# Optimization experiments

Measured on AMD Instinct MI355X. Metric: run time of the kernel, lower is better.

## Reference

```python
import jax, jax.numpy as jnp
import numpy as np

HIDDEN = 64
NUM_LAYERS = 6
BN_EPS = 1e-5


def setup_inputs() -> dict:
    key = jax.random.key(0)
    N, M = 1024, 1024
    num_nodes = N + M
    ks = jax.random.split(key, 12)
    x = jax.random.normal(ks[0], (num_nodes, 2), dtype=jnp.float32)
    # complete bipartite edges: (a, N+b) for all a in [0,N), b in [0,M), row-major so view(N,M) is meaningful
    row = jnp.repeat(jnp.arange(N, dtype=jnp.int64), M)
    col = N + jnp.tile(jnp.arange(M, dtype=jnp.int64), N)
    edge_index = jnp.stack([row, col], axis=0)
    s = 1.0 / np.sqrt(HIDDEN)
    return {
        "x": x,
        "edge_index": edge_index,
        "in_w": jax.random.normal(ks[1], (2, HIDDEN), jnp.float32) * 0.5,
        "in_b": jnp.zeros((HIDDEN,), jnp.float32),
        "conv_w": jax.random.normal(ks[2], (NUM_LAYERS, HIDDEN, HIDDEN), jnp.float32) * s,
        "conv_b": jnp.zeros((NUM_LAYERS, HIDDEN), jnp.float32),
        "bn_gamma": jnp.ones((NUM_LAYERS, HIDDEN), jnp.float32),
        "bn_beta": jnp.zeros((NUM_LAYERS, HIDDEN), jnp.float32),
        "out_w": jax.random.normal(ks[3], (2 * HIDDEN, 1), jnp.float32) * s,
        "out_b": jnp.zeros((1,), jnp.float32),
        "N": N,
        "M": M,
    }


def reference(x, edge_index, in_w, in_b, conv_w, conv_b, bn_gamma, bn_beta, out_w, out_b, N, M):
    num_nodes = x.shape[0]
    # GCN normalization with added self-loops (PyG GCNConv defaults)
    loops = jnp.arange(num_nodes, dtype=edge_index.dtype)
    row = jnp.concatenate([edge_index[0], loops])
    col = jnp.concatenate([edge_index[1], loops])
    deg = jax.ops.segment_sum(jnp.ones_like(col, dtype=x.dtype), col, num_segments=num_nodes)
    dinv = jnp.where(deg > 0, jax.lax.rsqrt(deg), 0.0)
    norm = dinv[row] * dinv[col]  # [E+num_nodes]

    h = jax.nn.relu(x @ in_w + in_b)
    for i in range(NUM_LAYERS):
        h_res = h
        hw = h @ conv_w[i]
        agg = jax.ops.segment_sum(hw[row] * norm[:, None], col, num_segments=num_nodes)
        h = agg + conv_b[i]
        # BatchNorm1d in training mode: batch stats, biased variance
        mu = h.mean(axis=0)
        var = ((h - mu) ** 2).mean(axis=0)
        h = (h - mu) * jax.lax.rsqrt(var + BN_EPS) * bn_gamma[i] + bn_beta[i]
        h = jax.nn.relu(h)
        if i > 0 and i % 2 == 1:
            h = h + h_res

    ef = jnp.concatenate([h[edge_index[0]], h[edge_index[1]]], axis=1)  # [E, 2H]
    scores = (ef @ out_w + out_b)[:, 0]
    return scores.reshape(N, M)
```

## Files before the change

kernel.cpp:

```cpp
#include <hip/hip_runtime.h>


#define NBLK 64
#define MAGIC 0x13572468u

__device__ __forceinline__ float relu_(float x) { return x > 0.f ? x : 0.f; }

#define AT_LOAD(p)    __hip_atomic_load((p), __ATOMIC_RELAXED, __HIP_MEMORY_SCOPE_AGENT)
#define AT_STORE(p,v) __hip_atomic_store((p), (v), __ATOMIC_RELAXED, __HIP_MEMORY_SCOPE_AGENT)
#define AT_ADD(p,v)   __hip_atomic_fetch_add((p), (v), __ATOMIC_RELAXED, __HIP_MEMORY_SCOPE_AGENT)

#define PART_OFF  256
#define UV_OFF    12544
#define FLAG_OFF  14592

__global__ __launch_bounds__(256, 1) void k_fused(
    const float* __restrict__ x,
    const float* __restrict__ in_w, const float* __restrict__ in_b,
    const float* __restrict__ conv_w,
    const float* __restrict__ bn_g, const float* __restrict__ bn_b,
    const float* __restrict__ out_w,
    unsigned int* __restrict__ ws)
{
    __shared__ float Wl[2][4096];
    __shared__ float hl[32 * 68];
    __shared__ float sredS[4 * 64], sredQ[4 * 64];
    __shared__ float stat[256];
    __shared__ float pcoef[64], scoef[64];
    __shared__ float g_lds[384], b_lds[384];
    __shared__ float ow_lds[128];

    const int t = threadIdx.x, b = blockIdx.x;
    const int nl = t >> 3;
    const int fi = t & 7;
    const int f0 = fi * 8;
    const int node = b * 32 + nl;
    const bool isA = b < 32;
    float* part = (float*)(ws + PART_OFF);
    float* uv   = (float*)(ws + UV_OFF);

    {
        const float4* src = (const float4*)conv_w;
        float4* dst = (float4*)Wl[0];
        dst[t]       = src[t];
        dst[t + 256] = src[t + 256];
        dst[t + 512] = src[t + 512];
        dst[t + 768] = src[t + 768];
        for (int i = t; i < 384; i += 256) { g_lds[i] = bn_g[i]; b_lds[i] = bn_b[i]; }
        if (t < 128) ow_lds[t] = out_w[t];
    }

    if (b == 0) {
        for (int i = t; i < 192; i += 256) AT_STORE(ws + i, 0u);
        for (int i = t; i < 12288; i += 256) AT_STORE((unsigned*)part + i, 0u);
        asm volatile("s_waitcnt vmcnt(0)" ::: "memory");
        __syncthreads();
        if (t == 0) AT_STORE(ws + FLAG_OFF, MAGIC);
    }

    {
        float x0 = x[node * 2], x1 = x[node * 2 + 1];
#pragma unroll
        for (int j = 0; j < 8; j++) {
            int f = f0 + j;
            hl[nl * 68 + f] = relu_(fmaf(x0, in_w[f], fmaf(x1, in_w[64 + f], in_b[f])));
        }
    }
    __syncthreads();

    for (int layer = 0; layer < 6; layer++) {
        const float* Wb = Wl[layer & 1];
        float acc[8];
#pragma unroll
        for (int j = 0; j < 8; j++) acc[j] = 0.f;

#pragma unroll 4
        for (int k = 0; k < 64; k += 4) {
            float4 hh = *(const float4*)&hl[nl * 68 + k];
            float hv[4] = {hh.x, hh.y, hh.z, hh.w};
#pragma unroll
            for (int j = 0; j < 4; j++) {
                const float* wr = Wb + (k + j) * 64 + f0;
                float4 w0 = *(const float4*)wr;
                float4 w1 = *(const float4*)(wr + 4);
                float wv[8] = {w0.x, w0.y, w0.z, w0.w, w1.x, w1.y, w1.z, w1.w};
#pragma unroll
                for (int q = 0; q < 8; q++) acc[q] = fmaf(hv[j], wv[q], acc[q]);
            }
        }

        {
            float sv[8], qv[8];
#pragma unroll
            for (int j = 0; j < 8; j++) { sv[j] = acc[j]; qv[j] = acc[j] * acc[j]; }
#pragma unroll
            for (int m = 8; m < 64; m <<= 1) {
#pragma unroll
                for (int j = 0; j < 8; j++) {
                    sv[j] += __shfl_xor(sv[j], m);
                    qv[j] += __shfl_xor(qv[j], m);
                }
            }
            int w = t >> 6, lane = t & 63;
            if (lane < 8) {
#pragma unroll
                for (int j = 0; j < 8; j++) {
                    sredS[w * 64 + lane * 8 + j] = sv[j];
                    sredQ[w * 64 + lane * 8 + j] = qv[j];
                }
            }
        }
        if (layer == 0) {
            __syncthreads();
            if (t == 0) while (AT_LOAD(ws + FLAG_OFF) != MAGIC) {}
        }
        __syncthreads();

        if (t < 64) {
            float S = sredS[t] + sredS[64 + t] + sredS[128 + t] + sredS[192 + t];
            float Q = sredQ[t] + sredQ[64 + t] + sredQ[128 + t] + sredQ[192 + t];
            float* base = part + layer * 2048 + (b & 7) * 256 + (isA ? 0 : 128);
            AT_ADD(base + t, S);
            AT_ADD(base + 64 + t, Q);
        }

        asm volatile("s_waitcnt vmcnt(0)" ::: "memory");
        __syncthreads();
        if (t == 0) AT_ADD(ws + layer * 32, 1u);

        float4 pf0, pf1, pf2, pf3;
        if (layer < 5) {
            const float4* src = (const float4*)(conv_w + (layer + 1) * 4096);
            pf0 = src[t];
            pf1 = src[t + 256];
            pf2 = src[t + 512];
            pf3 = src[t + 768];
        }

        if (t == 0) {
            const unsigned int* c = ws + layer * 32;
            for (;;) {
                unsigned a0 = AT_LOAD(c);
                unsigned a1 = AT_LOAD(c);
                unsigned a2 = AT_LOAD(c);
                unsigned a3 = AT_LOAD(c);
                if (a0 >= NBLK) break;
                if (a1 >= NBLK) break;
                if (a2 >= NBLK) break;
                if (a3 >= NBLK) break;
            }
        }
        __syncthreads();

        {
            int item = t;
            const float* p = part + layer * 2048 + item;
            float s = 0.f;
#pragma unroll
            for (int r = 0; r < 8; r++) s += AT_LOAD(p + r * 256);
            stat[item] = s;
        }

        if (layer < 5) {
            float4* dst = (float4*)Wl[(layer + 1) & 1];
            dst[t]       = pf0;
            dst[t + 256] = pf1;
            dst[t + 512] = pf2;
            dst[t + 768] = pf3;
        }
        __syncthreads();

        if (t < 64) {
            float SA = stat[t], QA = stat[64 + t], SB = stat[128 + t], QB = stat[192 + t];
            const float c1 = 9.75609756097561e-4f;
            const float c2 = 3.1234752377721214e-2f;
            float sumAgg = SA + c1 * SB + 1024.f * c2 * SA;
            float sumSq  = QA + c1 * c1 * QB + 2.f * c1 * c2 * SA * SB
                         + 1024.f * c2 * c2 * SA * SA;
            float meanAgg = sumAgg * (1.f / 2048.f);
            float var = sumSq * (1.f / 2048.f) - meanAgg * meanAgg;
            float rstd = rsqrtf(var + 1e-5f);
            float scale = rstd * g_lds[layer * 64 + t];
            float bt = b_lds[layer * 64 + t];
            if (isA) { pcoef[t] = scale;      scoef[t] = bt - meanAgg * scale; }
            else     { pcoef[t] = c1 * scale; scoef[t] = bt + (c2 * SA - meanAgg) * scale; }
        }
        __syncthreads();

        float vals[8];
#pragma unroll
        for (int j = 0; j < 8; j++)
            vals[j] = relu_(fmaf(acc[j], pcoef[f0 + j], scoef[f0 + j]));
        if (layer == 1 || layer == 3 || layer == 5) {
#pragma unroll
            for (int j = 0; j < 8; j++) vals[j] += hl[nl * 68 + f0 + j];
        }

        if (layer < 5) {
#pragma unroll
            for (int j = 0; j < 8; j++) hl[nl * 68 + f0 + j] = vals[j];
            __syncthreads();
        } else {
            const float* w = ow_lds + (isA ? 0 : 64) + f0;
            float d = 0.f;
#pragma unroll
            for (int j = 0; j < 8; j++) d = fmaf(vals[j], w[j], d);
            d += __shfl_xor(d, 1);
            d += __shfl_xor(d, 2);
            d += __shfl_xor(d, 4);
            if (fi == 0) AT_STORE(uv + node, d);
        }
    }
}

__global__ __launch_bounds__(256) void k_out(const float* __restrict__ uv,
                                             const float* __restrict__ out_b,
                                             float* __restrict__ out) {
    const int a = blockIdx.x;
    const int t = threadIdx.x;
    float ua = uv[a] + out_b[0];
    float4 vv = ((const float4*)(uv + 1024))[t];
    ((float4*)(out + a * 1024))[t] =
        make_float4(ua + vv.x, ua + vv.y, ua + vv.z, ua + vv.w);
}

extern "C" void kernel_launch(void* const* d_in, const int* in_sizes, int n_in,
                              void* d_out, int out_size, void* d_ws, size_t ws_size,
                              hipStream_t stream) {
    const float* x      = (const float*)d_in[0];
    const float* in_w   = (const float*)d_in[2];
    const float* in_b   = (const float*)d_in[3];
    const float* conv_w = (const float*)d_in[4];
    const float* bn_g   = (const float*)d_in[6];
    const float* bn_b   = (const float*)d_in[7];
    const float* out_w  = (const float*)d_in[8];
    const float* out_b  = (const float*)d_in[9];
    float* out = (float*)d_out;

    unsigned int* ws = (unsigned int*)d_ws;
    const float* uv = (const float*)(ws + UV_OFF);

    k_fused<<<NBLK, 256, 0, stream>>>(x, in_w, in_b, conv_w, bn_g, bn_b,
                                      out_w, ws);
    k_out<<<1024, 256, 0, stream>>>(uv, out_b, out);
}
```

Before: 113.7 us.

## Split-K GEMM across waves with LDS reduction and single-wave epilogue

The per-layer 32x64x64 matmul is repartitioned so each wave handles a quarter of the K dimension for all 32 nodes, with each thread covering 4 nodes x 8 features. Waves 1-3 write partial sums to a swizzled LDS buffer, and wave 0 reduces them. Wave 0 alone then computes the BN statistics, issues the global atomics, waits at the grid barrier and applies the epilogue. The hidden-state buffer uses an XOR-swizzled layout instead of padding. The aim is more register reuse of the weight loads and fewer block-wide barriers around the atomics, at the cost of an extra LDS reduction pass and more serialized atomics per thread in a single wave.

```diff
diff --git a/kernel.cpp b/kernel.cpp
--- a/kernel.cpp
+++ b/kernel.cpp
@@ -23,18 +23,21 @@
     unsigned int* __restrict__ ws)
 {
     __shared__ float Wl[2][4096];
-    __shared__ float hl[32 * 68];
-    __shared__ float sredS[4 * 64], sredQ[4 * 64];
+    __shared__ float hl[2048];
+    __shared__ float Pp[3 * 2048];
     __shared__ float stat[256];
-    __shared__ float pcoef[64], scoef[64];
     __shared__ float g_lds[384], b_lds[384];
     __shared__ float ow_lds[128];
 
     const int t = threadIdx.x, b = blockIdx.x;
-    const int nl = t >> 3;
-    const int fi = t & 7;
-    const int f0 = fi * 8;
-    const int node = b * 32 + nl;
+    const int w    = t >> 6;
+    const int lane = t & 63;
+    const int fi   = lane & 7;
+    const int f0   = fi * 8;
+    const int ng   = lane >> 3;
+    const int n0   = ng * 4;
+    const int sw   = ng & 3;
+    const int kb   = w * 16;
     const bool isA = b < 32;
     float* part = (float*)(ws + PART_OFF);
     float* uv   = (float*)(ws + UV_OFF);
@@ -59,40 +62,92 @@
     }
 
     {
+        const int nl = t >> 3, fj = (t & 7) * 8;
+        const int rsw = (nl >> 2) & 3;
+        const int node = b * 32 + nl;
         float x0 = x[node * 2], x1 = x[node * 2 + 1];
 #pragma unroll
         for (int j = 0; j < 8; j++) {
-            int f = f0 + j;
-            hl[nl * 68 + f] = relu_(fmaf(x0, in_w[f], fmaf(x1, in_w[64 + f], in_b[f])));
+            int f = fj + j;
+            float v = relu_(fmaf(x0, in_w[f], fmaf(x1, in_w[64 + f], in_b[f])));
+            hl[nl * 64 + ((((f >> 2)) ^ rsw) << 2) + (f & 3)] = v;
         }
     }
     __syncthreads();
 
     for (int layer = 0; layer < 6; layer++) {
         const float* Wb = Wl[layer & 1];
-        float acc[8];
-#pragma unroll
-        for (int j = 0; j < 8; j++) acc[j] = 0.f;
-
-#pragma unroll 4
-        for (int k = 0; k < 64; k += 4) {
-            float4 hh = *(const float4*)&hl[nl * 68 + k];
-            float hv[4] = {hh.x, hh.y, hh.z, hh.w};
+        float acc[4][8];
+#pragma unroll
+        for (int n = 0; n < 4; n++)
+#pragma unroll
+            for (int j = 0; j < 8; j++) acc[n][j] = 0.f;
+
+#pragma unroll
+        for (int kk = 0; kk < 16; kk += 4) {
+            const int cb = (kb + kk) >> 2;
+            float hv[4][4];
+#pragma unroll
+            for (int n = 0; n < 4; n++) {
+                float4 h4 = *(const float4*)&hl[(n0 + n) * 64 + ((cb ^ sw) << 2)];
+                hv[n][0] = h4.x; hv[n][1] = h4.y; hv[n][2] = h4.z; hv[n][3] = h4.w;
+            }
 #pragma unroll
             for (int j = 0; j < 4; j++) {
-                const float* wr = Wb + (k + j) * 64 + f0;
+                const float* wr = Wb + (kb + kk + j) * 64 + f0;
                 float4 w0 = *(const float4*)wr;
                 float4 w1 = *(const float4*)(wr + 4);
                 float wv[8] = {w0.x, w0.y, w0.z, w0.w, w1.x, w1.y, w1.z, w1.w};
 #pragma unroll
-                for (int q = 0; q < 8; q++) acc[q] = fmaf(hv[j], wv[q], acc[q]);
-            }
-        }
-
-        {
+                for (int n = 0; n < 4; n++)
+#pragma unroll
+                    for (int q = 0; q < 8; q++)
+                        acc[n][q] = fmaf(hv[n][j], wv[q], acc[n][q]);
+            }
+        }
+
+        float4 pf0, pf1, pf2, pf3;
+
+        if (w > 0) {
+            if (layer < 5) {
+                const float4* src = (const float4*)(conv_w + (layer + 1) * 4096);
+                pf0 = src[t];
+                pf1 = src[t + 256];
+                pf2 = src[t + 512];
+                pf3 = src[t + 768];
+            }
+            float* Pw = Pp + (w - 1) * 2048;
+#pragma unroll
+            for (int n = 0; n < 4; n++) {
+                float* prow = Pw + (n0 + n) * 64;
+                *(float4*)&prow[((2 * fi)     ^ sw) << 2] =
+                    make_float4(acc[n][0], acc[n][1], acc[n][2], acc[n][3]);
+                *(float4*)&prow[((2 * fi + 1) ^ sw) << 2] =
+                    make_float4(acc[n][4], acc[n][5], acc[n][6], acc[n][7]);
+            }
+        }
+        __syncthreads();
+
+        if (w == 0) {
+#pragma unroll
+            for (int r = 0; r < 3; r++) {
+                const float* Pr = Pp + r * 2048;
+#pragma unroll
+                for (int n = 0; n < 4; n++) {
+                    const float* prow = Pr + (n0 + n) * 64;
+                    float4 p0 = *(const float4*)&prow[((2 * fi)     ^ sw) << 2];
+                    float4 p1 = *(const float4*)&prow[((2 * fi + 1) ^ sw) << 2];
+                    acc[n][0] += p0.x; acc[n][1] += p0.y; acc[n][2] += p0.z; acc[n][3] += p0.w;
+                    acc[n][4] += p1.x; acc[n][5] += p1.y; acc[n][6] += p1.z; acc[n][7] += p1.w;
+                }
+            }
             float sv[8], qv[8];
 #pragma unroll
-            for (int j = 0; j < 8; j++) { sv[j] = acc[j]; qv[j] = acc[j] * acc[j]; }
+            for (int j = 0; j < 8; j++) {
+                sv[j] = (acc[0][j] + acc[1][j]) + (acc[2][j] + acc[3][j]);
+                qv[j] = fmaf(acc[0][j], acc[0][j], fmaf(acc[1][j], acc[1][j],
+                        fmaf(acc[2][j], acc[2][j], acc[3][j] * acc[3][j])));
+            }
 #pragma unroll
             for (int m = 8; m < 64; m <<= 1) {
 #pragma unroll
@@ -101,66 +156,47 @@
                     qv[j] += __shfl_xor(qv[j], m);
                 }
             }
-            int w = t >> 6, lane = t & 63;
-            if (lane < 8) {
+            if (layer == 0) { while (AT_LOAD(ws + FLAG_OFF) != MAGIC) {} }
+            if (ng == 0) {
+                float* base = part + layer * 2048 + (b & 7) * 256 + (isA ? 0 : 128) + f0;
 #pragma unroll
                 for (int j = 0; j < 8; j++) {
-                    sredS[w * 64 + lane * 8 + j] = sv[j];
-                    sredQ[w * 64 + lane * 8 + j] = qv[j];
-                }
-            }
-        }
-        if (layer == 0) {
-            __syncthreads();
-            if (t == 0) while (AT_LOAD(ws + FLAG_OFF) != MAGIC) {}
-        }
-        __syncthreads();
-
-        if (t < 64) {
-            float S = sredS[t] + sredS[64 + t] + sredS[128 + t] + sredS[192 + t];
-            float Q = sredQ[t] + sredQ[64 + t] + sredQ[128 + t] + sredQ[192 + t];
-            float* base = part + layer * 2048 + (b & 7) * 256 + (isA ? 0 : 128);
-            AT_ADD(base + t, S);
-            AT_ADD(base + 64 + t, Q);
-        }
-
-        asm volatile("s_waitcnt vmcnt(0)" ::: "memory");
-        __syncthreads();
-        if (t == 0) AT_ADD(ws + layer * 32, 1u);
-
-        float4 pf0, pf1, pf2, pf3;
-        if (layer < 5) {
-            const float4* src = (const float4*)(conv_w + (layer + 1) * 4096);
-            pf0 = src[t];
-            pf1 = src[t + 256];
-            pf2 = src[t + 512];
-            pf3 = src[t + 768];
-        }
-
-        if (t == 0) {
-            const unsigned int* c = ws + layer * 32;
-            for (;;) {
-                unsigned a0 = AT_LOAD(c);
-                unsigned a1 = AT_LOAD(c);
-                unsigned a2 = AT_LOAD(c);
-                unsigned a3 = AT_LOAD(c);
-                if (a0 >= NBLK) break;
-                if (a1 >= NBLK) break;
-                if (a2 >= NBLK) break;
-                if (a3 >= NBLK) break;
+                    AT_ADD(base + j, sv[j]);
+                    AT_ADD(base + 64 + j, qv[j]);
+                }
+            }
+            asm volatile("s_waitcnt vmcnt(0)" ::: "memory");
+            if (lane == 0) AT_ADD(ws + layer * 32, 1u);
+            if (layer < 5) {
+                const float4* src = (const float4*)(conv_w + (layer + 1) * 4096);
+                pf0 = src[t];
+                pf1 = src[t + 256];
+                pf2 = src[t + 512];
+                pf3 = src[t + 768];
+            }
+            if (t == 0) {
+                const unsigned int* c = ws + layer * 32;
+                for (;;) {
+                    unsigned a0 = AT_LOAD(c);
+                    unsigned a1 = AT_LOAD(c);
+                    unsigned a2 = AT_LOAD(c);
+                    unsigned a3 = AT_LOAD(c);
+                    if (a0 >= NBLK) break;
+                    if (a1 >= NBLK) break;
+                    if (a2 >= NBLK) break;
+                    if (a3 >= NBLK) break;
+                }
             }
         }
         __syncthreads();
 
         {
-            int item = t;
-            const float* p = part + layer * 2048 + item;
+            const float* p = part + layer * 2048 + t;
             float s = 0.f;
 #pragma unroll
             for (int r = 0; r < 8; r++) s += AT_LOAD(p + r * 256);
-            stat[item] = s;
-        }
-
+            stat[t] = s;
+        }
         if (layer < 5) {
             float4* dst = (float4*)Wl[(layer + 1) & 1];
             dst[t]       = pf0;
@@ -170,46 +206,90 @@
         }
         __syncthreads();
 
-        if (t < 64) {
-            float SA = stat[t], QA = stat[64 + t], SB = stat[128 + t], QB = stat[192 + t];
-            const float c1 = 9.75609756097561e-4f;
-            const float c2 = 3.1234752377721214e-2f;
-            float sumAgg = SA + c1 * SB + 1024.f * c2 * SA;
-            float sumSq  = QA + c1 * c1 * QB + 2.f * c1 * c2 * SA * SB
-                         + 1024.f * c2 * c2 * SA * SA;
-            float meanAgg = sumAgg * (1.f / 2048.f);
-            float var = sumSq * (1.f / 2048.f) - meanAgg * meanAgg;
-            float rstd = rsqrtf(var + 1e-5f);
-            float scale = rstd * g_lds[layer * 64 + t];
-            float bt = b_lds[layer * 64 + t];
-            if (isA) { pcoef[t] = scale;      scoef[t] = bt - meanAgg * scale; }
-            else     { pcoef[t] = c1 * scale; scoef[t] = bt + (c2 * SA - meanAgg) * scale; }
-        }
-        __syncthreads();
-
-        float vals[8];
-#pragma unroll
-        for (int j = 0; j < 8; j++)
-            vals[j] = relu_(fmaf(acc[j], pcoef[f0 + j], scoef[f0 + j]));
-        if (layer == 1 || layer == 3 || layer == 5) {
-#pragma unroll
-            for (int j = 0; j < 8; j++) vals[j] += hl[nl * 68 + f0 + j];
-        }
-
-        if (layer < 5) {
-#pragma unroll
-            for (int j = 0; j < 8; j++) hl[nl * 68 + f0 + j] = vals[j];
-            __syncthreads();
-        } else {
-            const float* w = ow_lds + (isA ? 0 : 64) + f0;
-            float d = 0.f;
-#pragma unroll
-            for (int j = 0; j < 8; j++) d = fmaf(vals[j], w[j], d);
-            d += __shfl_xor(d, 1);
-            d += __shfl_xor(d, 2);
-            d += __shfl_xor(d, 4);
-            if (fi == 0) AT_STORE(uv + node, d);
-        }
+        if (w == 0) {
+            float pc[8], sc[8];
+            {
+                float4 sa0 = *(const float4*)&stat[f0];
+                float4 sa1 = *(const float4*)&stat[f0 + 4];
+                float4 qa0 = *(const float4*)&stat[64 + f0];
+                float4 qa1 = *(const float4*)&stat[64 + f0 + 4];
+                float4 sb0 = *(const float4*)&stat[128 + f0];
+                float4 sb1 = *(const float4*)&stat[128 + f0 + 4];
+                float4 qb0 = *(const float4*)&stat[192 + f0];
+                float4 qb1 = *(const float4*)&stat[192 + f0 + 4];
+                float4 gg0 = *(const float4*)&g_lds[layer * 64 + f0];
+                float4 gg1 = *(const float4*)&g_lds[layer * 64 + f0 + 4];
+                float4 bb0 = *(const float4*)&b_lds[layer * 64 + f0];
+                float4 bb1 = *(const float4*)&b_lds[layer * 64 + f0 + 4];
+                float SA[8] = {sa0.x, sa0.y, sa0.z, sa0.w, sa1.x, sa1.y, sa1.z, sa1.w};
+                float QA[8] = {qa0.x, qa0.y, qa0.z, qa0.w, qa1.x, qa1.y, qa1.z, qa1.w};
+                float SB[8] = {sb0.x, sb0.y, sb0.z, sb0.w, sb1.x, sb1.y, sb1.z, sb1.w};
+                float QB[8] = {qb0.x, qb0.y, qb0.z, qb0.w, qb1.x, qb1.y, qb1.z, qb1.w};
+                float GG[8] = {gg0.x, gg0.y, gg0.z, gg0.w, gg1.x, gg1.y, gg1.z, gg1.w};
+                float BB[8] = {bb0.x, bb0.y, bb0.z, bb0.w, bb1.x, bb1.y, bb1.z, bb1.w};
+                const float c1 = 9.75609756097561e-4f;
+                const float c2 = 3.1234752377721214e-2f;
+#pragma unroll
+                for (int j = 0; j < 8; j++) {
+                    float sumAgg = SA[j] + c1 * SB[j] + 1024.f * c2 * SA[j];
+                    float sumSq  = QA[j] + c1 * c1 * QB[j] + 2.f * c1 * c2 * SA[j] * SB[j]
+                                 + 1024.f * c2 * c2 * SA[j] * SA[j];
+                    float meanAgg = sumAgg * (1.f / 2048.f);
+                    float var = sumSq * (1.f / 2048.f) - meanAgg * meanAgg;
+                    float rstd = rsqrtf(var + 1e-5f);
+                    float scale = rstd * GG[j];
+                    if (isA) { pc[j] = scale;      sc[j] = BB[j] - meanAgg * scale; }
+                    else     { pc[j] = c1 * scale; sc[j] = BB[j] + (c2 * SA[j] - meanAgg) * scale; }
+                }
+            }
+            float vals[4][8];
+#pragma unroll
+            for (int n = 0; n < 4; n++)
+#pragma unroll
+                for (int j = 0; j < 8; j++)
+                    vals[n][j] = relu_(fmaf(acc[n][j], pc[j], sc[j]));
+            if (layer == 1 || layer == 3 || layer == 5) {
+#pragma unroll
+                for (int n = 0; n < 4; n++) {
+                    const float* hrow = hl + (n0 + n) * 64;
+                    float4 r0 = *(const float4*)&hrow[((2 * fi)     ^ sw) << 2];
+                    float4 r1 = *(const float4*)&hrow[((2 * fi + 1) ^ sw) << 2];
+                    vals[n][0] += r0.x; vals[n][1] += r0.y; vals[n][2] += r0.z; vals[n][3] += r0.w;
+                    vals[n][4] += r1.x; vals[n][5] += r1.y; vals[n][6] += r1.z; vals[n][7] += r1.w;
+                }
+            }
+            if (layer < 5) {
+#pragma unroll
+                for (int n = 0; n < 4; n++) {
+                    float* hrow = hl + (n0 + n) * 64;
+                    *(float4*)&hrow[((2 * fi)     ^ sw) << 2] =
+                        make_float4(vals[n][0], vals[n][1], vals[n][2], vals[n][3]);
+                    *(float4*)&hrow[((2 * fi + 1) ^ sw) << 2] =
+                        make_float4(vals[n][4], vals[n][5], vals[n][6], vals[n][7]);
+                }
+            } else {
+                const float* wv = ow_lds + (isA ? 0 : 64) + f0;
+                float4 o0 = *(const float4*)wv;
+                float4 o1 = *(const float4*)(wv + 4);
+                float d[4];
+#pragma unroll
+                for (int n = 0; n < 4; n++) {
+                    d[n] = fmaf(vals[n][0], o0.x, fmaf(vals[n][1], o0.y,
+                           fmaf(vals[n][2], o0.z, fmaf(vals[n][3], o0.w,
+                           fmaf(vals[n][4], o1.x, fmaf(vals[n][5], o1.y,
+                           fmaf(vals[n][6], o1.z, vals[n][7] * o1.w)))))));
+                    d[n] += __shfl_xor(d[n], 1);
+                    d[n] += __shfl_xor(d[n], 2);
+                    d[n] += __shfl_xor(d[n], 4);
+                }
+                if (fi == 0) {
+#pragma unroll
+                    for (int n = 0; n < 4; n++)
+                        AT_STORE(uv + b * 32 + n0 + n, d[n]);
+                }
+            }
+        }
+        __syncthreads();
     }
 }
 
```

Measured after the change: 118.6 us. 1.04x slower.
